# Optimization experiments

Measured on AMD Instinct MI355X. Metric: run time of the kernel, lower is better.

Reference implementation:

```python
import jax, jax.numpy as jnp
import numpy as np

N_HEAD = 16
D_MODEL = 1024
D_HEAD = D_MODEL // N_HEAD
B, T = 2, 2048


def setup_inputs() -> dict:
    key = jax.random.key(0)
    k1, k2, k3 = jax.random.split(key, 3)
    x = jax.random.normal(k1, (B, T, D_MODEL), dtype=jnp.float32)
    w_attn = jax.random.normal(k2, (3 * D_MODEL, D_MODEL), dtype=jnp.float32) * (D_MODEL ** -0.5)
    w_proj = jax.random.normal(k3, (D_MODEL, D_MODEL), dtype=jnp.float32) * (D_MODEL ** -0.5)
    return {"x": x, "w_attn": w_attn, "w_proj": w_proj}


def _rms_norm(x):
    eps = jnp.asarray(jnp.finfo(x.dtype).eps, x.dtype)
    var = jnp.mean(jnp.square(x), axis=-1, keepdims=True)
    return x * jax.lax.rsqrt(var + eps)


def _rotate_half(x):
    x1, x2 = jnp.split(x, 2, axis=-1)
    return jnp.concatenate((-x2, x1), axis=-1)


def reference(x, w_attn, w_proj):
    Bx, Tx, C = x.shape
    qkv = jnp.einsum('btc,fc->btf', x, w_attn)  # [B,T,3C]
    q, k, v = jnp.split(qkv, 3, axis=-1)
    # [B, H, T, Dh]
    q = q.reshape(Bx, Tx, N_HEAD, D_HEAD).transpose(0, 2, 1, 3)
    k = k.reshape(Bx, Tx, N_HEAD, D_HEAD).transpose(0, 2, 1, 3)
    v = v.reshape(Bx, Tx, N_HEAD, D_HEAD).transpose(0, 2, 1, 3)
    # QK RMSNorm (no learned weight)
    q = _rms_norm(q)
    k = _rms_norm(k)
    # Rotary embedding over full d_head: freqs tiled twice
    inv_freq = 1.0 / (10000.0 ** (jnp.arange(0, D_HEAD, 2, dtype=jnp.float32) / D_HEAD))
    t = jnp.arange(Tx, dtype=jnp.float32)
    freqs = jnp.einsum('i,j->ij', t, inv_freq)  # [T, Dh/2]
    emb = jnp.concatenate((freqs, freqs), axis=-1)  # [T, Dh]
    cos = jnp.cos(emb)[None, None, :, :]
    sin = jnp.sin(emb)[None, None, :, :]
    q = q * cos + _rotate_half(q) * sin
    k = k * cos + _rotate_half(k) * sin
    # Causal SDPA
    scale = D_HEAD ** -0.5
    scores = jnp.einsum('bhqd,bhkd->bhqk', q, k) * scale
    causal = jnp.tril(jnp.ones((Tx, Tx), dtype=bool))
    scores = jnp.where(causal[None, None], scores, jnp.asarray(-jnp.inf, scores.dtype))
    attn = jax.nn.softmax(scores, axis=-1)
    y = jnp.einsum('bhqk,bhkd->bhqd', attn, v)
    y = y.transpose(0, 2, 1, 3).reshape(Bx, Tx, C)
    return jnp.einsum('btc,oc->bto', y, w_proj)
```

## Files before the change

kernel.cpp:

```cpp
#include <hip/hip_runtime.h>
#include <cstdint>
#include <cstddef>


typedef short bf16x8 __attribute__((ext_vector_type(8)));
typedef short bf16x4 __attribute__((ext_vector_type(4)));
typedef float floatx4 __attribute__((ext_vector_type(4)));
typedef float floatx2 __attribute__((ext_vector_type(2)));
typedef unsigned short ushortx8 __attribute__((ext_vector_type(8)));
typedef unsigned short ushortx4 __attribute__((ext_vector_type(4)));
typedef unsigned int uintx2 __attribute__((ext_vector_type(2)));

#define DEVI __device__ __forceinline__

DEVI unsigned short f2bf(float f) {
    unsigned int u = __builtin_bit_cast(unsigned int, f);
    u += 0x7fffu + ((u >> 16) & 1u);
    return (unsigned short)(u >> 16);
}
DEVI unsigned int pkbf2(float a, float b) {
    unsigned int ua = __builtin_bit_cast(unsigned int, a) + 0x8000u;
    unsigned int ub = __builtin_bit_cast(unsigned int, b) + 0x8000u;
    return __builtin_amdgcn_perm(ub, ua, 0x07060302);
}

DEVI void glds16(const unsigned short* g, unsigned short* l) {
    __builtin_amdgcn_global_load_lds(
        (const __attribute__((address_space(1))) unsigned int*)g,
        (__attribute__((address_space(3))) unsigned int*)l, 16, 0, 0);
}

DEVI void cast8(unsigned short* dst, const float* src) {
    floatx4 a = *(const floatx4*)src;
    floatx4 b = *(const floatx4*)(src + 4);
    ushortx8 o;
    o[0] = f2bf(a[0]); o[1] = f2bf(a[1]); o[2] = f2bf(a[2]); o[3] = f2bf(a[3]);
    o[4] = f2bf(b[0]); o[5] = f2bf(b[1]); o[6] = f2bf(b[2]); o[7] = f2bf(b[3]);
    *(ushortx8*)dst = o;
}

__global__ __launch_bounds__(256)
void cast_inputs(const float* __restrict__ x, const float* __restrict__ wa,
                 const float* __restrict__ wp,
                 unsigned short* __restrict__ xb, unsigned short* __restrict__ wab,
                 unsigned short* __restrict__ wpb, float* __restrict__ ropetab)
{
    size_t g = (size_t)blockIdx.x * 256 + threadIdx.x;
    size_t stride = (size_t)gridDim.x * 256;
    for (size_t i = g; i < (4194304 / 8); i += stride) cast8(xb  + i * 8, x  + i * 8);
    for (size_t i = g; i < (3145728 / 8); i += stride) cast8(wab + i * 8, wa + i * 8);
    for (size_t i = g; i < (1048576 / 8); i += stride) cast8(wpb + i * 8, wp + i * 8);
    for (size_t i = g; i < 65536; i += stride) {
        int t = (int)(i >> 5), f = (int)(i & 31);
        float ang = (float)t * __expf(-(float)f * 0.28782313662425572f);
        float sn, cs;
        __sincosf(ang, &sn, &cs);
        ropetab[2 * i]     = cs;
        ropetab[2 * i + 1] = sn;
    }
}

__global__ __launch_bounds__(512, 2)
void gemm_qkv_8ph(const unsigned short* __restrict__ A,
                  const unsigned short* __restrict__ B,
                  const float* __restrict__ ropetab,
                  unsigned short* __restrict__ Cqk,
                  unsigned short* __restrict__ Vt)
{
    __shared__ __align__(16) unsigned short lds[2][2][256 * 64];

    const int tid  = threadIdx.x;
    const int lane = tid & 63;
    const int w    = tid >> 6;
    const int wm   = w >> 2;
    const int wn   = w & 3;
    const int quad = lane >> 4;
    const int lm   = lane & 15;

    const int lin = blockIdx.y * 12 + blockIdx.x;
    const int s   = (lin & 7) * 24 + (lin >> 3);
    const int m0  = (s / 12) * 256;
    const int n0  = (s % 12) * 256;

    const int srow = tid >> 3;
    const int scol = (((tid & 7) ^ ((tid >> 3) & 7)) * 8);
    const int ldst = w * 512;

#define STG_A(u, WBi, kq) glds16(&A[(size_t)(m0 + (u) * 64 + srow) * 1024 + (kq) + scol], \
                                 &lds[WBi][0][(u) * 4096 + ldst])
#define STG_B(u, WBi, kq) glds16(&B[(size_t)(n0 + (u) * 64 + srow) * 1024 + (kq) + scol], \
                                 &lds[WBi][1][(u) * 4096 + ldst])
#define RD_A(RBi, rrow, kk) (*(const bf16x8*)&lds[RBi][0][(rrow) * 64 + ((((kk) * 4 + quad) ^ ((rrow) & 7)) * 8)])
#define RD_B(RBi, rrow, kk) (*(const bf16x8*)&lds[RBi][1][(rrow) * 64 + ((((kk) * 4 + quad) ^ ((rrow) & 7)) * 8)])

    floatx4 acc[8][4] = {};
    bf16x8 afr[4][2];
    bf16x8 bfr[4][2];

#define MQ(MB, JB)                                                              \
  do {                                                                          \
    _Pragma("unroll")                                                           \
    for (int kk = 0; kk < 2; ++kk)                                              \
      _Pragma("unroll")                                                         \
      for (int mi = 0; mi < 4; ++mi)                                            \
        _Pragma("unroll")                                                       \
        for (int j2 = 0; j2 < 2; ++j2)                                          \
          acc[(MB) + mi][(JB) + j2] = __builtin_amdgcn_mfma_f32_16x16x32_bf16(  \
              afr[mi][kk], bfr[(JB) + j2][kk], acc[(MB) + mi][(JB) + j2], 0, 0, 0); \
  } while (0)

#define TILE(RBi, WBi, KT, LASTF)                                               \
  do {                                                                          \
    const int kn = ((KT) + 1) * 64;                                             \
    if (!(LASTF)) { STG_B(0, WBi, kn); STG_B(1, WBi, kn); }                     \
    _Pragma("unroll")                                                           \
    for (int kk = 0; kk < 2; ++kk) {                                            \
      _Pragma("unroll")                                                         \
      for (int mi = 0; mi < 4; ++mi)                                            \
        afr[mi][kk] = RD_A(RBi, wm * 128 + mi * 16 + lm, kk);                   \
      _Pragma("unroll")                                                         \
      for (int j2 = 0; j2 < 2; ++j2)                                            \
        bfr[j2][kk] = RD_B(RBi, wn * 64 + j2 * 16 + lm, kk);                    \
    }                                                                           \
    asm volatile("s_waitcnt lgkmcnt(8)" ::: "memory");                          \
    __builtin_amdgcn_s_barrier();                                               \
    asm volatile("s_waitcnt lgkmcnt(0)" ::: "memory");                          \
    __builtin_amdgcn_s_setprio(1); MQ(0, 0); __builtin_amdgcn_s_setprio(0);     \
    __builtin_amdgcn_s_barrier();                                               \
    if (!(LASTF)) { STG_B(2, WBi, kn); STG_B(3, WBi, kn); }                     \
    _Pragma("unroll")                                                           \
    for (int kk = 0; kk < 2; ++kk)                                              \
      _Pragma("unroll")                                                         \
      for (int j2 = 0; j2 < 2; ++j2)                                            \
        bfr[2 + j2][kk] = RD_B(RBi, wn * 64 + (2 + j2) * 16 + lm, kk);          \
    if (!(LASTF)) { asm volatile("s_waitcnt vmcnt(4)" ::: "memory"); }          \
    else          { asm volatile("s_waitcnt vmcnt(0)" ::: "memory"); }          \
    __builtin_amdgcn_s_barrier();                                               \
    asm volatile("s_waitcnt lgkmcnt(0)" ::: "memory");                          \
    __builtin_amdgcn_s_setprio(1); MQ(0, 2); __builtin_amdgcn_s_setprio(0);     \
    __builtin_amdgcn_s_barrier();                                               \
    if (!(LASTF)) { STG_A(0, WBi, kn); STG_A(2, WBi, kn); }                     \
    _Pragma("unroll")                                                           \
    for (int kk = 0; kk < 2; ++kk)                                              \
      _Pragma("unroll")                                                         \
      for (int mi = 0; mi < 4; ++mi)                                            \
        afr[mi][kk] = RD_A(RBi, wm * 128 + 64 + mi * 16 + lm, kk);              \
    __builtin_amdgcn_s_barrier();                                               \
    asm volatile("s_waitcnt lgkmcnt(0)" ::: "memory");                          \
    __builtin_amdgcn_s_setprio(1); MQ(4, 2); __builtin_amdgcn_s_setprio(0);     \
    __builtin_amdgcn_s_barrier();                                               \
    if (!(LASTF)) { STG_A(1, WBi, kn); STG_A(3, WBi, kn);                       \
                    asm volatile("s_waitcnt vmcnt(2)" ::: "memory"); }          \
    __builtin_amdgcn_s_barrier();                                               \
    __builtin_amdgcn_s_setprio(1); MQ(4, 0); __builtin_amdgcn_s_setprio(0);     \
    __builtin_amdgcn_s_barrier();                                               \
  } while (0)

    STG_B(0, 0, 0); STG_B(1, 0, 0); STG_B(2, 0, 0); STG_B(3, 0, 0);
    STG_A(0, 0, 0); STG_A(2, 0, 0); STG_A(1, 0, 0); STG_A(3, 0, 0);
    asm volatile("s_waitcnt vmcnt(2)" ::: "memory");
    __builtin_amdgcn_s_barrier();

    for (int kt = 0; kt < 14; kt += 2) {
        TILE(0, 1, kt, false);
        TILE(1, 0, kt + 1, false);
    }
    TILE(0, 1, 14, false);
    TILE(1, 0, 15, true);

    const bool is_v = (n0 + wn * 64) >= 2048;
    if (!is_v) {
        const float qsc = ((n0 + wn * 64) < 1024) ? 0.18033688011112043f : 1.0f;
        const floatx2* rtab = (const floatx2*)ropetab;
        #pragma unroll
        for (int mi = 0; mi < 8; ++mi) {
            float rn[4];
            #pragma unroll
            for (int r = 0; r < 4; ++r) {
                float ss = 0.0f;
                #pragma unroll
                for (int j = 0; j < 4; ++j) ss += acc[mi][j][r] * acc[mi][j][r];
                ss += __shfl_xor(ss, 1, 64);
                ss += __shfl_xor(ss, 2, 64);
                ss += __shfl_xor(ss, 4, 64);
                ss += __shfl_xor(ss, 8, 64);
                rn[r] = rsqrtf(ss * (1.0f / 64.0f) + 1.1920929e-07f);
            }
            #pragma unroll
            for (int r = 0; r < 4; ++r) {
                int row = m0 + wm * 128 + mi * 16 + quad * 4 + r;
                int t = row & 2047;
                floatx2 cs0 = rtab[t * 32 + lm];
                floatx2 cs1 = rtab[t * 32 + 16 + lm];
                float g = rn[r];
                #pragma unroll
                for (int j = 0; j < 4; ++j) {
                    int d = j * 16 + lm;
                    float cs = (j & 1) ? cs1[0] : cs0[0];
                    float sn = (j & 1) ? cs1[1] : cs0[1];
                    float v  = acc[mi][j][r] * g;
                    float vp = acc[mi][j ^ 2][r] * g;
                    float sgn = (d < 32) ? -1.0f : 1.0f;
                    Cqk[(size_t)row * 2048 + (n0 + wn * 64 + d)] =
                        f2bf((v * cs + sgn * vp * sn) * qsc);
                }
            }
        }
    } else {
        #pragma unroll
        for (int mi = 0; mi < 8; ++mi)
            #pragma unroll
            for (int j = 0; j < 4; ++j) {
                int col  = n0 + wn * 64 + j * 16 + lm;
                int row0 = m0 + wm * 128 + mi * 16 + quad * 4;
                int bq = row0 >> 11, t0 = row0 & 2047;
                ushortx4 pk;
                #pragma unroll
                for (int r = 0; r < 4; ++r) pk[r] = f2bf(acc[mi][j][r]);
                *(ushortx4*)&Vt[((size_t)(bq * 1024 + (col - 2048))) * 2048 + t0] = pk;
            }
    }
#undef TILE
#undef MQ
#undef RD_A
#undef RD_B
#undef STG_A
#undef STG_B
}

template <int BN, int BK>
__global__ __launch_bounds__(256)
void gemm_bt(const unsigned short* __restrict__ A, const unsigned short* __restrict__ B,
             float* __restrict__ Cf, int M, int N, int K)
{
    constexpr int WCOLS = (BN == 128) ? 2 : 1;
    constexpr int WROWS = 4 / WCOLS;
    constexpr int MI    = 128 / (16 * WROWS);
    constexpr int LPR   = BK / 8;
    constexpr int RPI   = 64 / LPR;

    __shared__ __align__(16) unsigned short As[128 * BK];
    __shared__ __align__(16) unsigned short Bs[BN * BK];

    const int tid  = threadIdx.x;
    const int lane = tid & 63;
    const int w    = tid >> 6;
    const int wm   = w / WCOLS, wn = w % WCOLS;
    const int quad = lane >> 4;
    const int lm   = lane & 15;
    const int m0 = blockIdx.y * 128;
    const int n0 = blockIdx.x * BN;
    const int sr = lane / LPR;
    const int sc = (lane % LPR) * 8;

    floatx4 acc[MI][4] = {};

    for (int k0 = 0; k0 < K; k0 += BK) {
        __syncthreads();
        #pragma unroll
        for (int i = 0; i < 32 / RPI; ++i) {
            int r = w * 32 + i * RPI;
            glds16(&A[(size_t)(m0 + r + sr) * K + k0 + sc], &As[r * BK]);
        }
        #pragma unroll
        for (int i = 0; i < (BN / 4) / RPI; ++i) {
            int r = w * (BN / 4) + i * RPI;
            glds16(&B[(size_t)(n0 + r + sr) * K + k0 + sc], &Bs[r * BK]);
        }
        __syncthreads();

        #pragma unroll
        for (int kk = 0; kk < BK / 32; ++kk) {
            bf16x8 a[MI];
            #pragma unroll
            for (int i = 0; i < MI; ++i)
                a[i] = *(const bf16x8*)&As[(wm * (16 * MI) + i * 16 + lm) * BK + kk * 32 + quad * 8];
            #pragma unroll
            for (int j = 0; j < 4; ++j) {
                bf16x8 b = *(const bf16x8*)&Bs[(wn * 64 + j * 16 + lm) * BK + kk * 32 + quad * 8];
                #pragma unroll
                for (int i = 0; i < MI; ++i)
                    acc[i][j] = __builtin_amdgcn_mfma_f32_16x16x32_bf16(a[i], b, acc[i][j], 0, 0, 0);
            }
        }
    }

    #pragma unroll
    for (int i = 0; i < MI; ++i)
        #pragma unroll
        for (int j = 0; j < 4; ++j) {
            int col  = n0 + wn * 64 + j * 16 + lm;
            int row0 = m0 + wm * (16 * MI) + i * 16 + quad * 4;
            #pragma unroll
            for (int r = 0; r < 4; ++r)
                Cf[(size_t)(row0 + r) * N + col] = acc[i][j][r];
        }
}

#define GRP(OT, LT, QT, g, KT, DG)                                             \
  {                                                                            \
    floatx4 sa = {};                                                           \
    sa = __builtin_amdgcn_mfma_f32_16x16x32_bf16(kf0, QT[0], sa, 0, 0, 0);     \
    sa = __builtin_amdgcn_mfma_f32_16x16x32_bf16(kf1, QT[1], sa, 0, 0, 0);     \
    float p0 = exp2f(sa[0]);                                                   \
    float p1 = exp2f(sa[1]);                                                   \
    float p2 = exp2f(sa[2]);                                                   \
    float p3 = exp2f(sa[3]);                                                   \
    if (DG) {                                                                  \
      int kb = (KT) * 64 + w * 16 + quad * 4;                                  \
      int qr = q0 + (g) * 16 + lm;                                             \
      if (kb + 0 > qr) p0 = 0.0f;                                              \
      if (kb + 1 > qr) p1 = 0.0f;                                              \
      if (kb + 2 > qr) p2 = 0.0f;                                              \
      if (kb + 3 > qr) p3 = 0.0f;                                              \
    }                                                                          \
    uintx2 pk;                                                                 \
    pk[0] = pkbf2(p0, p1);                                                     \
    pk[1] = pkbf2(p2, p3);                                                     \
    bf16x4 pa = __builtin_bit_cast(bf16x4, pk);                                \
    LT = __builtin_amdgcn_mfma_f32_16x16x16bf16_1k(pa, ones4, LT, 0, 0, 0);    \
    OT[0] = __builtin_amdgcn_mfma_f32_16x16x16bf16_1k(pa, vb0, OT[0], 0, 0, 0);\
    OT[1] = __builtin_amdgcn_mfma_f32_16x16x16bf16_1k(pa, vb1, OT[1], 0, 0, 0);\
    OT[2] = __builtin_amdgcn_mfma_f32_16x16x16bf16_1k(pa, vb2, OT[2], 0, 0, 0);\
    OT[3] = __builtin_amdgcn_mfma_f32_16x16x16bf16_1k(pa, vb3, OT[3], 0, 0, 0);\
  }

#define ATTN_STEP(KS, VS, KSn, VSn, KT, DG, LAST)                              \
  do {                                                                         \
    if (!(LAST)) {                                                             \
      const size_t tn = (size_t)((KT) + 1);                                    \
      glds16(kg + tn * 131072,         (KSn) + w * 512);                       \
      glds16(kg + tn * 131072 + 65536, (KSn) + 2048 + w * 512);                \
      glds16(vg + tn * 64,             (VSn) + w * 512);                       \
      glds16(vg + tn * 64 + 65536,     (VSn) + 2048 + w * 512);                \
    }                                                                          \
    bf16x8 kf0 = *(const bf16x8*)&(KS)[kfo0];                                  \
    bf16x8 kf1 = *(const bf16x8*)&(KS)[kfo1];                                  \
    bf16x4 vb0 = *(const bf16x4*)&(VS)[vbo0];                                  \
    bf16x4 vb1 = *(const bf16x4*)&(VS)[vbo1];                                  \
    bf16x4 vb2 = *(const bf16x4*)&(VS)[vbo2];                                  \
    bf16x4 vb3 = *(const bf16x4*)&(VS)[vbo3];                                  \
    GRP(oA, lA, qfA, 0, KT, DG)                                                \
    GRP(oB, lB, qfB, 1, KT, DG)                                                \
    GRP(oC, lC, qfC, 2, KT, DG)                                                \
    GRP(oD, lD, qfD, 3, KT, DG)                                                \
    if (!(LAST)) __syncthreads();                                              \
  } while (0)

#define OWR1(S, OT, g)                                                         \
  _Pragma("unroll")                                                            \
  for (int jd = 0; jd < 4; ++jd)                                               \
    _Pragma("unroll")                                                          \
    for (int r = 0; r < 4; ++r)                                                \
      (S)[((g) * 16 + quad * 4 + r) * 64 + jd * 16 + lm] = OT[jd][r];
#define OWR(S) { OWR1(S, oA, 0) OWR1(S, oB, 1) OWR1(S, oC, 2) OWR1(S, oD, 3) }
#define OAC1(S, OT, g)                                                         \
  _Pragma("unroll")                                                            \
  for (int jd = 0; jd < 4; ++jd)                                               \
    _Pragma("unroll")                                                          \
    for (int r = 0; r < 4; ++r)                                                \
      OT[jd][r] += (S)[((g) * 16 + quad * 4 + r) * 64 + jd * 16 + lm];
#define OAC(S) { OAC1(S, oA, 0) OAC1(S, oB, 1) OAC1(S, oC, 2) OAC1(S, oD, 3) }

#define YWR(OT, g)                                                             \
  {                                                                            \
    float rv[4];                                                               \
    _Pragma("unroll")                                                          \
    for (int r = 0; r < 4; ++r) {                                              \
      int qi = (g) * 16 + quad * 4 + r;                                        \
      rv[r] = 1.0f / (lsc[qi] + lsc[64 + qi] + lsc[128 + qi] + lsc[192 + qi]); \
    }                                                                          \
    _Pragma("unroll")                                                          \
    for (int jd = 0; jd < 4; ++jd)                                             \
      _Pragma("unroll")                                                        \
      for (int r = 0; r < 4; ++r)                                              \
        Y[((size_t)(b * 2048 + q0 + (g) * 16 + quad * 4 + r)) * 1024 +         \
          h * 64 + jd * 16 + lm] = f2bf(OT[jd][r] * rv[r]);                    \
  }

__global__ __launch_bounds__(256, 2)
void attention(const unsigned short* __restrict__ qk,
               const unsigned short* __restrict__ Vt,
               unsigned short* __restrict__ Y)
{
    __shared__ __align__(16) unsigned short smem[20480];
    unsigned short* const QPs = smem;
    unsigned short* const Ks0 = smem + 4096;
    unsigned short* const Ks1 = smem + 8192;
    unsigned short* const Vs0 = smem + 12288;
    unsigned short* const Vs1 = smem + 16384;
    float* const lsc  = (float*)smem;
    float* const ScrA = (float*)(smem + 4096);
    float* const ScrB = (float*)(smem + 12288);

    const int tid  = threadIdx.x;
    const int lane = tid & 63;
    const int w    = tid >> 6;
    const int quad = lane >> 4;
    const int lm   = lane & 15;
    const int sx   = lm & 7;

    const int bh = blockIdx.x;
    const int qt = 31 - blockIdx.y;
    const int b  = bh >> 4, h = bh & 15;
    const int q0 = qt * 64;

    const int kfo0 = (w * 16 + lm) * 64 + ((quad)     ^ sx) * 8;
    const int kfo1 = (w * 16 + lm) * 64 + ((4 + quad) ^ sx) * 8;
    const int vch  = (w * 2 + (quad >> 1)) ^ sx;
    const int vbo0 = (0 * 16 + lm) * 64 + vch * 8 + (quad & 1) * 4;
    const int vbo1 = (1 * 16 + lm) * 64 + vch * 8 + (quad & 1) * 4;
    const int vbo2 = (2 * 16 + lm) * 64 + vch * 8 + (quad & 1) * 4;
    const int vbo3 = (3 * 16 + lm) * 64 + vch * 8 + (quad & 1) * 4;

    const int srow = tid >> 3;
    const int scol = ((tid & 7) ^ (srow & 7)) * 8;
    const unsigned short* kg = qk + (size_t)b * 4194304 + 1024 + h * 64
                             + (size_t)srow * 2048 + scol;
    const unsigned short* vg = Vt + (size_t)bh * 131072 + (size_t)srow * 2048 + scol;
    const unsigned short* qg = qk + ((size_t)(b * 2048 + q0 + srow)) * 2048
                             + h * 64 + scol;

    glds16(qg,         QPs + w * 512);
    glds16(qg + 65536, QPs + 2048 + w * 512);
    glds16(kg,         Ks0 + w * 512);
    glds16(kg + 65536, Ks0 + 2048 + w * 512);
    glds16(vg,         Vs0 + w * 512);
    glds16(vg + 65536, Vs0 + 2048 + w * 512);
    __syncthreads();

    bf16x8 qfA[2], qfB[2], qfC[2], qfD[2];
    #pragma unroll
    for (int kk = 0; kk < 2; ++kk) {
        qfA[kk] = *(const bf16x8*)&QPs[(0 * 16 + lm) * 64 + ((kk * 4 + quad) ^ sx) * 8];
        qfB[kk] = *(const bf16x8*)&QPs[(1 * 16 + lm) * 64 + ((kk * 4 + quad) ^ sx) * 8];
        qfC[kk] = *(const bf16x8*)&QPs[(2 * 16 + lm) * 64 + ((kk * 4 + quad) ^ sx) * 8];
        qfD[kk] = *(const bf16x8*)&QPs[(3 * 16 + lm) * 64 + ((kk * 4 + quad) ^ sx) * 8];
    }

    bf16x4 ones4;
    #pragma unroll
    for (int i = 0; i < 4; ++i) ones4[i] = (short)0x3F80;

    floatx4 oA[4] = {}, oB[4] = {}, oC[4] = {}, oD[4] = {};
    floatx4 lA = {}, lB = {}, lC = {}, lD = {};

    int kt = 0;
    for (; kt + 1 < qt; kt += 2) {
        ATTN_STEP(Ks0, Vs0, Ks1, Vs1, kt,     false, false);
        ATTN_STEP(Ks1, Vs1, Ks0, Vs0, kt + 1, false, false);
    }
    if (kt < qt) {
        ATTN_STEP(Ks0, Vs0, Ks1, Vs1, kt, false, false);
        ATTN_STEP(Ks1, Vs1, Ks0, Vs0, qt, true, true);
    } else {
        ATTN_STEP(Ks0, Vs0, Ks1, Vs1, qt, true, true);
    }

    __syncthreads();
    if (lm == 0) {
        #pragma unroll
        for (int r = 0; r < 4; ++r) {
            lsc[w * 64 +  0 + quad * 4 + r] = lA[r];
            lsc[w * 64 + 16 + quad * 4 + r] = lB[r];
            lsc[w * 64 + 32 + quad * 4 + r] = lC[r];
            lsc[w * 64 + 48 + quad * 4 + r] = lD[r];
        }
    }
    if (w == 1) { OWR(ScrA) }
    if (w == 3) { OWR(ScrB) }
    __syncthreads();
    if (w == 0) { OAC(ScrA) }
    if (w == 2) { OAC(ScrB) }
    __syncthreads();
    if (w == 2) { OWR(ScrA) }
    __syncthreads();
    if (w == 0) {
        OAC(ScrA)
        YWR(oA, 0)
        YWR(oB, 1)
        YWR(oC, 2)
        YWR(oD, 3)
    }
}

extern "C" void kernel_launch(void* const* d_in, const int* in_sizes, int n_in,
                              void* d_out, int out_size, void* d_ws, size_t ws_size,
                              hipStream_t stream)
{
    const float* x      = (const float*)d_in[0];
    const float* w_attn = (const float*)d_in[1];
    const float* w_proj = (const float*)d_in[2];
    float* out = (float*)d_out;

    unsigned short* qkbuf = (unsigned short*)d_ws;
    unsigned short* Vtb   = qkbuf + (size_t)4096 * 2048;
    unsigned short* y     = Vtb   + (size_t)32 * 64 * 2048;
    unsigned short* wpb   = y     + (size_t)4096 * 1024;
    unsigned short* xb  = (unsigned short*)d_out;
    unsigned short* wab = xb + (size_t)4096 * 1024;
    float* ropetab = (float*)(wab + (size_t)3072 * 1024);

    dim3 blk(256);
    cast_inputs<<<dim3(1024), blk, 0, stream>>>(x, w_attn, w_proj, xb, wab, wpb, ropetab);
    gemm_qkv_8ph<<<dim3(12, 16), dim3(512), 0, stream>>>(xb, wab, ropetab, qkbuf, Vtb);
    attention<<<dim3(32, 32), blk, 0, stream>>>(qkbuf, Vtb, y);
    gemm_bt<64, 64>
        <<<dim3(16, 32), blk, 0, stream>>>(y, wpb, out, 4096, 1024, 1024);
}
```

Before: 177.7 us.

## Split long causal query tiles across two blocks with a partial-sum reduce

Long query tiles (qt>=16) are split into two key-range halves processed by separate blocks, using a constant work-item table ordered roughly by descending length. Each half writes unnormalized fp32 outputs and row sums to scratch, and a new reduce kernel combines them into the bf16 output. This evens out the triangular causal workload across 48 block slots per head. In exchange it adds an extra kernel launch and fp32 partial-result traffic, and the scratch overlaps d_out and the workspace. It relies on the exp2 path without a running max, so summing partials without rescaling stays consistent.

```diff
diff --git a/kernel.cpp b/kernel.cpp
--- a/kernel.cpp
+++ b/kernel.cpp
@@ -297,6 +297,21 @@
         }
 }
 
+#define ENC(qt, t0, nt) ((qt) | ((t0) << 8) | ((nt) << 16))
+__constant__ int g_items[48] = {
+    ENC(31,0,16), ENC(31,16,16), ENC(30,0,16), ENC(15,0,16),
+    ENC(30,16,15), ENC(29,0,15), ENC(29,15,15), ENC(28,0,15), ENC(14,0,15),
+    ENC(28,15,14), ENC(27,0,14), ENC(27,14,14), ENC(26,0,14), ENC(13,0,14),
+    ENC(26,14,13), ENC(25,0,13), ENC(25,13,13), ENC(24,0,13), ENC(12,0,13),
+    ENC(24,13,12), ENC(23,0,12), ENC(23,12,12), ENC(22,0,12), ENC(11,0,12),
+    ENC(22,12,11), ENC(21,0,11), ENC(21,11,11), ENC(20,0,11), ENC(10,0,11),
+    ENC(20,11,10), ENC(19,0,10), ENC(19,10,10), ENC(18,0,10), ENC(9,0,10),
+    ENC(18,10,9),  ENC(17,0,9),  ENC(17,9,9),   ENC(16,0,9),  ENC(8,0,9),
+    ENC(16,9,8),   ENC(7,0,8),
+    ENC(6,0,7), ENC(5,0,6), ENC(4,0,5), ENC(3,0,4), ENC(2,0,3), ENC(1,0,2),
+    ENC(0,0,1)
+};
+
 #define GRP(OT, LT, QT, g, KT, DG)                                             \
   {                                                                            \
     floatx4 sa = {};                                                           \
@@ -378,10 +393,24 @@
           h * 64 + jd * 16 + lm] = f2bf(OT[jd][r] * rv[r]);                    \
   }
 
+#define PWR(OT, g)                                                             \
+  {                                                                            \
+    _Pragma("unroll")                                                          \
+    for (int r = 0; r < 4; ++r) {                                              \
+      int qi = (g) * 16 + quad * 4 + r;                                        \
+      if (lm == 0)                                                             \
+        pl[qi] = lsc[qi] + lsc[64 + qi] + lsc[128 + qi] + lsc[192 + qi];       \
+      _Pragma("unroll")                                                        \
+      for (int jd = 0; jd < 4; ++jd)                                           \
+        po[qi * 64 + jd * 16 + lm] = OT[jd][r];                                \
+    }                                                                          \
+  }
+
 __global__ __launch_bounds__(256, 2)
 void attention(const unsigned short* __restrict__ qk,
                const unsigned short* __restrict__ Vt,
-               unsigned short* __restrict__ Y)
+               unsigned short* __restrict__ Y,
+               float* __restrict__ Po, float* __restrict__ Pl)
 {
     __shared__ __align__(16) unsigned short smem[20480];
     unsigned short* const QPs = smem;
@@ -401,9 +430,14 @@
     const int sx   = lm & 7;
 
     const int bh = blockIdx.x;
-    const int qt = 31 - blockIdx.y;
+    const int it = g_items[blockIdx.y];
+    const int qt = it & 255;
+    const int t0 = (it >> 8) & 255;
+    const int nt = it >> 16;
     const int b  = bh >> 4, h = bh & 15;
     const int q0 = qt * 64;
+    const bool mflag   = (t0 + nt - 1) == qt;
+    const bool partial = qt >= 16;
 
     const int kfo0 = (w * 16 + lm) * 64 + ((quad)     ^ sx) * 8;
     const int kfo1 = (w * 16 + lm) * 64 + ((4 + quad) ^ sx) * 8;
@@ -423,10 +457,10 @@
 
     glds16(qg,         QPs + w * 512);
     glds16(qg + 65536, QPs + 2048 + w * 512);
-    glds16(kg,         Ks0 + w * 512);
-    glds16(kg + 65536, Ks0 + 2048 + w * 512);
-    glds16(vg,         Vs0 + w * 512);
-    glds16(vg + 65536, Vs0 + 2048 + w * 512);
+    glds16(kg + (size_t)t0 * 131072,         Ks0 + w * 512);
+    glds16(kg + (size_t)t0 * 131072 + 65536, Ks0 + 2048 + w * 512);
+    glds16(vg + t0 * 64,         Vs0 + w * 512);
+    glds16(vg + t0 * 64 + 65536, Vs0 + 2048 + w * 512);
     __syncthreads();
 
     bf16x8 qfA[2], qfB[2], qfC[2], qfD[2];
@@ -445,16 +479,16 @@
     floatx4 oA[4] = {}, oB[4] = {}, oC[4] = {}, oD[4] = {};
     floatx4 lA = {}, lB = {}, lC = {}, lD = {};
 
-    int kt = 0;
-    for (; kt + 1 < qt; kt += 2) {
-        ATTN_STEP(Ks0, Vs0, Ks1, Vs1, kt,     false, false);
-        ATTN_STEP(Ks1, Vs1, Ks0, Vs0, kt + 1, false, false);
-    }
-    if (kt < qt) {
-        ATTN_STEP(Ks0, Vs0, Ks1, Vs1, kt, false, false);
-        ATTN_STEP(Ks1, Vs1, Ks0, Vs0, qt, true, true);
+    int ct = 0;
+    for (; ct + 2 < nt; ct += 2) {
+        ATTN_STEP(Ks0, Vs0, Ks1, Vs1, t0 + ct,     false, false);
+        ATTN_STEP(Ks1, Vs1, Ks0, Vs0, t0 + ct + 1, false, false);
+    }
+    if (ct + 2 == nt) {
+        ATTN_STEP(Ks0, Vs0, Ks1, Vs1, t0 + ct,     false, false);
+        ATTN_STEP(Ks1, Vs1, Ks0, Vs0, t0 + ct + 1, mflag, true);
     } else {
-        ATTN_STEP(Ks0, Vs0, Ks1, Vs1, qt, true, true);
+        ATTN_STEP(Ks0, Vs0, Ks1, Vs1, t0 + ct, mflag, true);
     }
 
     __syncthreads();
@@ -477,10 +511,54 @@
     __syncthreads();
     if (w == 0) {
         OAC(ScrA)
-        YWR(oA, 0)
-        YWR(oB, 1)
-        YWR(oC, 2)
-        YWR(oD, 3)
+        if (!partial) {
+            YWR(oA, 0)
+            YWR(oB, 1)
+            YWR(oC, 2)
+            YWR(oD, 3)
+        } else {
+            const int pidx = (bh * 16 + (qt - 16)) * 2 + (t0 ? 1 : 0);
+            float* po = Po + (size_t)pidx * 4096;
+            float* pl = Pl + (size_t)pidx * 64;
+            PWR(oA, 0)
+            PWR(oB, 1)
+            PWR(oC, 2)
+            PWR(oD, 3)
+        }
+    }
+}
+
+__global__ __launch_bounds__(256)
+void attn_reduce(const float* __restrict__ Po, const float* __restrict__ Pl,
+                 unsigned short* __restrict__ Y)
+{
+    const int bh = blockIdx.x, qi = blockIdx.y;
+    const int b = bh >> 4, h = bh & 15;
+    const int q0 = (16 + qi) * 64;
+    const int tid = threadIdx.x;
+    const int row = tid >> 2;
+    const int c0  = (tid & 3) * 16;
+    const size_t base = ((size_t)(bh * 16 + qi)) * 2;
+    const float* po0 = Po + (base + 0) * 4096 + row * 64 + c0;
+    const float* po1 = Po + (base + 1) * 4096 + row * 64 + c0;
+    const float rinv = 1.0f / (Pl[(base + 0) * 64 + row] + Pl[(base + 1) * 64 + row]);
+    unsigned short* yp = Y + ((size_t)(b * 2048 + q0 + row)) * 1024 + h * 64 + c0;
+    #pragma unroll
+    for (int c = 0; c < 2; ++c) {
+        floatx4 a  = *(const floatx4*)(po0 + c * 8);
+        floatx4 a2 = *(const floatx4*)(po0 + c * 8 + 4);
+        floatx4 e  = *(const floatx4*)(po1 + c * 8);
+        floatx4 e2 = *(const floatx4*)(po1 + c * 8 + 4);
+        ushortx8 o;
+        o[0] = f2bf((a[0]  + e[0])  * rinv);
+        o[1] = f2bf((a[1]  + e[1])  * rinv);
+        o[2] = f2bf((a[2]  + e[2])  * rinv);
+        o[3] = f2bf((a[3]  + e[3])  * rinv);
+        o[4] = f2bf((a2[0] + e2[0]) * rinv);
+        o[5] = f2bf((a2[1] + e2[1]) * rinv);
+        o[6] = f2bf((a2[2] + e2[2]) * rinv);
+        o[7] = f2bf((a2[3] + e2[3]) * rinv);
+        *(ushortx8*)(yp + c * 8) = o;
     }
 }
 
@@ -497,14 +575,17 @@
     unsigned short* Vtb   = qkbuf + (size_t)4096 * 2048;
     unsigned short* y     = Vtb   + (size_t)32 * 64 * 2048;
     unsigned short* wpb   = y     + (size_t)4096 * 1024;
+    float* Plb            = (float*)(wpb + (size_t)1024 * 1024);
     unsigned short* xb  = (unsigned short*)d_out;
     unsigned short* wab = xb + (size_t)4096 * 1024;
     float* ropetab = (float*)(wab + (size_t)3072 * 1024);
+    float* Pob = (float*)d_out;
 
     dim3 blk(256);
     cast_inputs<<<dim3(1024), blk, 0, stream>>>(x, w_attn, w_proj, xb, wab, wpb, ropetab);
     gemm_qkv_8ph<<<dim3(12, 16), dim3(512), 0, stream>>>(xb, wab, ropetab, qkbuf, Vtb);
-    attention<<<dim3(32, 32), blk, 0, stream>>>(qkbuf, Vtb, y);
+    attention<<<dim3(32, 48), blk, 0, stream>>>(qkbuf, Vtb, y, Pob, Plb);
+    attn_reduce<<<dim3(32, 16), blk, 0, stream>>>(Pob, Plb, y);
     gemm_bt<64, 64>
         <<<dim3(16, 32), blk, 0, stream>>>(y, wpb, out, 4096, 1024, 1024);
 }
```

Measured after the change: 187.3 us. +5.4%, slower.

## Triple-buffer K/V tiles with prefetch distance two and partial vmcnt waits

Applied to the files above, without the earlier changes.

Moves attention's K/V staging from double to triple buffering in LDS, prefetching the tile two iterations ahead. The full __syncthreads is replaced with s_waitcnt vmcnt(4) plus s_barrier, so the newest loads stay in flight across the barrier. This aims to hide global-load latency better, at the cost of more LDS per block (56KB), which may reduce occupancy.

```diff
diff --git a/kernel.cpp b/kernel.cpp
--- a/kernel.cpp
+++ b/kernel.cpp
@@ -325,14 +325,15 @@
     OT[3] = __builtin_amdgcn_mfma_f32_16x16x16bf16_1k(pa, vb3, OT[3], 0, 0, 0);\
   }
 
-#define ATTN_STEP(KS, VS, KSn, VSn, KT, DG, LAST)                              \
+#define ATTN_STEP(KS, VS, KP, VP, KT, DG, LAST)                                \
   do {                                                                         \
-    if (!(LAST)) {                                                             \
-      const size_t tn = (size_t)((KT) + 1);                                    \
-      glds16(kg + tn * 131072,         (KSn) + w * 512);                       \
-      glds16(kg + tn * 131072 + 65536, (KSn) + 2048 + w * 512);                \
-      glds16(vg + tn * 64,             (VSn) + w * 512);                       \
-      glds16(vg + tn * 64 + 65536,     (VSn) + 2048 + w * 512);                \
+    const bool pf = (KT) + 2 <= qt;                                            \
+    if (pf) {                                                                  \
+      const size_t tn = (size_t)((KT) + 2);                                    \
+      glds16(kg + tn * 131072,         (KP) + w * 512);                        \
+      glds16(kg + tn * 131072 + 65536, (KP) + 2048 + w * 512);                 \
+      glds16(vg + tn * 64,             (VP) + w * 512);                        \
+      glds16(vg + tn * 64 + 65536,     (VP) + 2048 + w * 512);                 \
     }                                                                          \
     bf16x8 kf0 = *(const bf16x8*)&(KS)[kfo0];                                  \
     bf16x8 kf1 = *(const bf16x8*)&(KS)[kfo1];                                  \
@@ -344,7 +345,11 @@
     GRP(oB, lB, qfB, 1, KT, DG)                                                \
     GRP(oC, lC, qfC, 2, KT, DG)                                                \
     GRP(oD, lD, qfD, 3, KT, DG)                                                \
-    if (!(LAST)) __syncthreads();                                              \
+    if (!(LAST)) {                                                             \
+      if (pf) { asm volatile("s_waitcnt vmcnt(4)" ::: "memory"); }             \
+      else    { asm volatile("s_waitcnt vmcnt(0)" ::: "memory"); }             \
+      __builtin_amdgcn_s_barrier();                                            \
+    }                                                                          \
   } while (0)
 
 #define OWR1(S, OT, g)                                                         \
@@ -383,15 +388,17 @@
                const unsigned short* __restrict__ Vt,
                unsigned short* __restrict__ Y)
 {
-    __shared__ __align__(16) unsigned short smem[20480];
+    __shared__ __align__(16) unsigned short smem[28672];
     unsigned short* const QPs = smem;
     unsigned short* const Ks0 = smem + 4096;
     unsigned short* const Ks1 = smem + 8192;
-    unsigned short* const Vs0 = smem + 12288;
-    unsigned short* const Vs1 = smem + 16384;
+    unsigned short* const Ks2 = smem + 12288;
+    unsigned short* const Vs0 = smem + 16384;
+    unsigned short* const Vs1 = smem + 20480;
+    unsigned short* const Vs2 = smem + 24576;
     float* const lsc  = (float*)smem;
     float* const ScrA = (float*)(smem + 4096);
-    float* const ScrB = (float*)(smem + 12288);
+    float* const ScrB = (float*)(smem + 16384);
 
     const int tid  = threadIdx.x;
     const int lane = tid & 63;
@@ -404,6 +411,7 @@
     const int qt = 31 - blockIdx.y;
     const int b  = bh >> 4, h = bh & 15;
     const int q0 = qt * 64;
+    const int NT = qt + 1;
 
     const int kfo0 = (w * 16 + lm) * 64 + ((quad)     ^ sx) * 8;
     const int kfo1 = (w * 16 + lm) * 64 + ((4 + quad) ^ sx) * 8;
@@ -427,7 +435,16 @@
     glds16(kg + 65536, Ks0 + 2048 + w * 512);
     glds16(vg,         Vs0 + w * 512);
     glds16(vg + 65536, Vs0 + 2048 + w * 512);
-    __syncthreads();
+    if (qt >= 1) {
+        glds16(kg + 131072,         Ks1 + w * 512);
+        glds16(kg + 131072 + 65536, Ks1 + 2048 + w * 512);
+        glds16(vg + 64,             Vs1 + w * 512);
+        glds16(vg + 64 + 65536,     Vs1 + 2048 + w * 512);
+        asm volatile("s_waitcnt vmcnt(4)" ::: "memory");
+    } else {
+        asm volatile("s_waitcnt vmcnt(0)" ::: "memory");
+    }
+    __builtin_amdgcn_s_barrier();
 
     bf16x8 qfA[2], qfB[2], qfC[2], qfD[2];
     #pragma unroll
@@ -445,16 +462,24 @@
     floatx4 oA[4] = {}, oB[4] = {}, oC[4] = {}, oD[4] = {};
     floatx4 lA = {}, lB = {}, lC = {}, lD = {};
 
-    int kt = 0;
-    for (; kt + 1 < qt; kt += 2) {
-        ATTN_STEP(Ks0, Vs0, Ks1, Vs1, kt,     false, false);
-        ATTN_STEP(Ks1, Vs1, Ks0, Vs0, kt + 1, false, false);
-    }
-    if (kt < qt) {
-        ATTN_STEP(Ks0, Vs0, Ks1, Vs1, kt, false, false);
-        ATTN_STEP(Ks1, Vs1, Ks0, Vs0, qt, true, true);
-    } else {
-        ATTN_STEP(Ks0, Vs0, Ks1, Vs1, qt, true, true);
+    int t = 0;
+    for (; t + 3 < NT; t += 3) {
+        ATTN_STEP(Ks0, Vs0, Ks2, Vs2, t,     false, false);
+        ATTN_STEP(Ks1, Vs1, Ks0, Vs0, t + 1, false, false);
+        ATTN_STEP(Ks2, Vs2, Ks1, Vs1, t + 2, false, false);
+    }
+    {
+        const int r = NT - t;
+        if (r == 3) {
+            ATTN_STEP(Ks0, Vs0, Ks2, Vs2, t,     false, false);
+            ATTN_STEP(Ks1, Vs1, Ks0, Vs0, t + 1, false, false);
+            ATTN_STEP(Ks2, Vs2, Ks1, Vs1, qt,    true,  true);
+        } else if (r == 2) {
+            ATTN_STEP(Ks0, Vs0, Ks2, Vs2, t,  false, false);
+            ATTN_STEP(Ks1, Vs1, Ks0, Vs0, qt, true,  true);
+        } else {
+            ATTN_STEP(Ks0, Vs0, Ks2, Vs2, qt, true, true);
+        }
     }
 
     __syncthreads();
```

New measurement: 179.4 us. No clear change (+0.9%).
